# Optimization experiments

Measured on AMD Instinct MI355X. Metric: run time of the kernel, lower is better.

The kernel has to match this reference:

```python
import jax, jax.numpy as jnp
import numpy as np

STRIDES = (8.0, 16.0, 32.0)
ANCHORS = np.array([[[10, 13], [16, 30], [33, 23]],
                    [[30, 61], [62, 45], [59, 119]],
                    [[116, 90], [156, 198], [373, 326]]], dtype=np.float32)
NC = 80
NO = NC + 5
NA = 3
CONF_THRES = 0.15
IOU_THRES = 0.45
MAX_DET = 100
TOPK = 1000          # NMS candidate pre-selection (greedy NMS over top-1000 scores)
MASK_SIZE = 28
MAX_WH = 4096.0      # class offset for batched (class-aware) NMS


def conv(x, w):
    # NCHW conv, stride 1, 'SAME' padding == torch padding=k//2
    return jax.lax.conv_general_dilated(x, w, (1, 1), 'SAME',
                                        dimension_numbers=('NCHW', 'OIHW', 'NCHW'))


def convbn(x, w, g, b, act=False):
    # Conv + (folded) BatchNorm affine + optional SiLU
    y = conv(x, w) * g[None, :, None, None] + b[None, :, None, None]
    return y * jax.nn.sigmoid(y) if act else y


def resize_ac(x, oh, ow):
    # bilinear resize, align_corners=True, NCHW
    H, W = x.shape[-2], x.shape[-1]
    ys = jnp.linspace(0.0, H - 1.0, oh)
    xs = jnp.linspace(0.0, W - 1.0, ow)
    y0 = jnp.floor(ys).astype(jnp.int32); y1 = jnp.minimum(y0 + 1, H - 1)
    x0 = jnp.floor(xs).astype(jnp.int32); x1 = jnp.minimum(x0 + 1, W - 1)
    fy = ys - y0; fx = xs - x0
    rows = x[..., y0, :] * (1.0 - fy)[:, None] + x[..., y1, :] * fy[:, None]
    return rows[..., x0] * (1.0 - fx) + rows[..., x1] * fx


def decode(fraw, anchors_px, stride):
    # fraw: [bs, na*no, ny, nx] -> [bs, na*ny*nx, no] in pixel coords
    bs, _, ny, nx = fraw.shape
    d = fraw.reshape(bs, NA, NO, ny, nx).transpose(0, 1, 3, 4, 2)  # [bs,na,ny,nx,no]
    y = jax.nn.sigmoid(d)
    yv, xv = jnp.meshgrid(jnp.arange(ny, dtype=fraw.dtype),
                          jnp.arange(nx, dtype=fraw.dtype), indexing='ij')
    grid = jnp.stack((xv, yv), -1) - 0.5                 # [ny,nx,2]
    xy = (y[..., :2] * 2.0 + grid) * stride
    wh = (y[..., 2:4] * 2.0) ** 2 * anchors_px[None, :, None, None, :]
    return jnp.concatenate((xy, wh, y[..., 4:]), -1).reshape(bs, -1, NO)


def box_iou(a, b):
    area = lambda t: (t[:, 2] - t[:, 0]) * (t[:, 3] - t[:, 1])
    lt = jnp.maximum(a[:, None, :2], b[None, :, :2])
    rb = jnp.minimum(a[:, None, 2:], b[None, :, 2:])
    wh = jnp.clip(rb - lt, 0.0)
    inter = wh[..., 0] * wh[..., 1]
    return inter / (area(a)[:, None] + area(b)[None, :] - inter + 1e-7)


def nms_image(pred):
    # pred: [N, 85]. conf = obj * cls (multi_label=False -> best class)
    xy = pred[:, :2]; wh = pred[:, 2:4]
    boxes = jnp.concatenate((xy - wh / 2.0, xy + wh / 2.0), -1)
    obj = pred[:, 4]; cls = pred[:, 5:]
    score = obj * jnp.max(cls, -1)
    cls_idx = jnp.argmax(cls, -1)
    s = jnp.where(score > CONF_THRES, score, -1.0)
    sK, idx = jax.lax.top_k(s, TOPK)
    bK = boxes[idx]; cK = cls_idx[idx]
    vK = sK > CONF_THRES
    offb = bK + (cK.astype(bK.dtype) * MAX_WH)[:, None]  # class-aware offset
    iou = box_iou(offb, offb)

    def body(i, st):
        keep, supp = st
        ki = vK[i] & jnp.logical_not(supp[i])
        supp = jnp.where(ki, jnp.logical_or(supp, iou[i] > IOU_THRES), supp)
        return keep.at[i].set(ki), supp

    keep, _ = jax.lax.fori_loop(0, TOPK, body,
                                (jnp.zeros(TOPK, dtype=bool), jnp.zeros(TOPK, dtype=bool)))
    sF = jnp.where(keep, sK, -1.0)
    top_s, top_i = jax.lax.top_k(sF, MAX_DET)
    valid = top_s > 0.0
    out_boxes = bK[top_i] * valid[:, None]
    out_scores = jnp.where(valid, top_s, 0.0)
    out_labels = jnp.where(valid, cK[top_i] + 1, 0)  # 1-based labels
    return out_boxes, out_scores, out_labels, valid


def bilinear_sample(img, ys, xs):
    # img [C,H,W]; ys, xs [P] -> [C,P]; edge-clamped
    H, W = img.shape[-2], img.shape[-1]
    ys = jnp.clip(ys, 0.0, H - 1.0); xs = jnp.clip(xs, 0.0, W - 1.0)
    y0 = jnp.floor(ys).astype(jnp.int32); y1 = jnp.minimum(y0 + 1, H - 1)
    x0 = jnp.floor(xs).astype(jnp.int32); x1 = jnp.minimum(x0 + 1, W - 1)
    ly = ys - y0; lx = xs - x0
    v00 = img[:, y0, x0]; v01 = img[:, y0, x1]
    v10 = img[:, y1, x0]; v11 = img[:, y1, x1]
    return (v00 * (1 - ly) * (1 - lx) + v01 * (1 - ly) * lx +
            v10 * ly * (1 - lx) + v11 * ly * lx)


def roi_align(f, rois, b_idx, out=MASK_SIZE):
    # aligned=False, spatial_scale applied by caller, 1 sample per bin (bin center)
    frac = (jnp.arange(out, dtype=f.dtype) + 0.5) / out

    def one(b, box):
        img = f[b]
        x1, y1, x2, y2 = box[0], box[1], box[2], box[3]
        rw = jnp.maximum(x2 - x1, 1.0); rh = jnp.maximum(y2 - y1, 1.0)
        cx = x1 + frac * rw; cy = y1 + frac * rh
        ys = jnp.repeat(cy, out); xs = jnp.tile(cx, out)
        return bilinear_sample(img, ys, xs).reshape(-1, out, out)

    return jax.vmap(one)(b_idx, rois)


def forward(x0, x1, x2, w_det0, b_det0, w_det1, b_det1, w_det2, b_det2,
            w_seg0, g_seg0, b_seg0, w_seg1, g_seg1, b_seg1, w_seg2, g_seg2, b_seg2,
            w_sc, g_sc, b_sc, w_ml, b_ml):
    feats = (x0, x1, x2)
    wdet = ((w_det0, b_det0), (w_det1, b_det1), (w_det2, b_det2))
    preds = []
    for i in range(3):
        fraw = conv(feats[i], wdet[i][0]) + wdet[i][1][None, :, None, None]
        preds.append(decode(fraw, jnp.asarray(ANCHORS[i]), STRIDES[i]))
    preds = jnp.concatenate(preds, 1)  # [bs, 25200, 85]

    # seg FPN: top-down with align_corners=True bilinear upsample + add
    f = convbn(x2, w_seg0, g_seg0, b_seg0)
    f = resize_ac(f, x1.shape[-2], x1.shape[-1])
    f = convbn(f + x1, w_seg1, g_seg1, b_seg1)
    f = resize_ac(f, x0.shape[-2], x0.shape[-1])
    f = convbn(f + x0, w_seg2, g_seg2, b_seg2)  # [bs, 128, 80, 80]

    boxes, scores, labels, valid = jax.vmap(nms_image)(preds)
    bs = boxes.shape[0]
    rois = jax.lax.stop_gradient(boxes) / STRIDES[0]   # boxes.detach() / stride[0]
    b_idx = jnp.repeat(jnp.arange(bs), MAX_DET)
    crops = roi_align(f, rois.reshape(-1, 4), b_idx)   # [bs*MAX_DET, 128, 28, 28]

    # seg_h: SiLU -> Conv(k=3, act=True) -> 1x1 mask logits
    h = crops * jax.nn.sigmoid(crops)
    h = convbn(h, w_sc, g_sc, b_sc, act=True)
    logits = conv(h, w_ml) + b_ml[None, :, None, None]
    probs = jax.nn.sigmoid(logits)                     # [R, 80, 28, 28]
    lab = jnp.clip(labels.reshape(-1) - 1, 0, NC - 1)  # nc == nc_masks: pick class channel
    masks = probs[jnp.arange(probs.shape[0]), lab]
    masks = masks.reshape(bs, MAX_DET, MASK_SIZE, MASK_SIZE) * valid[..., None, None]
    return boxes, scores, labels, valid, masks


def setup_inputs() -> dict:
    key = jax.random.key(0)
    ks = iter(jax.random.split(key, 48))

    def rn(shape, scale=1.0):
        return jax.random.normal(next(ks), shape, jnp.float32) * scale

    def wconv(o, i, k):
        return rn((o, i, k, k), 1.0 / float(np.sqrt(i * k * k)))

    return {
        'x0': rn((2, 256, 80, 80)),
        'x1': rn((2, 512, 40, 40)),
        'x2': rn((2, 1024, 20, 20)),
        'w_det0': wconv(255, 256, 1), 'b_det0': rn((255,), 0.1),
        'w_det1': wconv(255, 512, 1), 'b_det1': rn((255,), 0.1),
        'w_det2': wconv(255, 1024, 1), 'b_det2': rn((255,), 0.1),
        'w_seg0': wconv(512, 1024, 3), 'g_seg0': jnp.ones(512, jnp.float32), 'b_seg0': rn((512,), 0.1),
        'w_seg1': wconv(256, 512, 3), 'g_seg1': jnp.ones(256, jnp.float32), 'b_seg1': rn((256,), 0.1),
        'w_seg2': wconv(128, 256, 3), 'g_seg2': jnp.ones(128, jnp.float32), 'b_seg2': rn((128,), 0.1),
        'w_sc': wconv(128, 128, 3), 'g_sc': jnp.ones(128, jnp.float32), 'b_sc': rn((128,), 0.1),
        'w_ml': wconv(80, 128, 1), 'b_ml': rn((80,), 0.1),
    }


def reference(x0, x1, x2, w_det0, b_det0, w_det1, b_det1, w_det2, b_det2,
              w_seg0, g_seg0, b_seg0, w_seg1, g_seg1, b_seg1, w_seg2, g_seg2, b_seg2,
              w_sc, g_sc, b_sc, w_ml, b_ml):
    return forward(x0, x1, x2, w_det0, b_det0, w_det1, b_det1, w_det2, b_det2,
                   w_seg0, g_seg0, b_seg0, w_seg1, g_seg1, b_seg1, w_seg2, g_seg2, b_seg2,
                   w_sc, g_sc, b_sc, w_ml, b_ml)
```

## Files before the change

### kernel.cpp

```cpp
#include <hip/hip_runtime.h>
#include <hip/hip_bf16.h>

typedef unsigned int u32;
typedef unsigned long long u64;
typedef short bf16x8 __attribute__((ext_vector_type(8)));
typedef float f32x4 __attribute__((ext_vector_type(4)));

#define NCAND 1000
#define NANCH 25200

__device__ __forceinline__ float sig_acc(float x) { return 1.0f / (1.0f + expf(-x)); }
__device__ __forceinline__ float silu_fast(float v) { return v / (1.0f + __expf(-v)); }
__device__ __forceinline__ unsigned short f2b(float f) {
    __hip_bfloat16 h = __float2bfloat16(f);
    return *reinterpret_cast<unsigned short*>(&h);
}
__device__ __forceinline__ float b2f(unsigned short u) {
    return __uint_as_float(((u32)u) << 16);
}
__device__ __forceinline__ int swz(int p) { return (p & 3) ^ ((p >> 2) & 3); }

__device__ __forceinline__ void gload16(const void* g, void* l) {
    __builtin_amdgcn_global_load_lds((const __attribute__((address_space(1))) void*)g,
                                     (__attribute__((address_space(3))) void*)l, 16, 0, 0);
// ... 70 lines not shown
        }
        __syncthreads();
        for (int k = t; k < 512; k += 256) {
            int pp = k >> 3, cg = k & 7;
            int gp = p0 + pp;
            if (gp < HW) {
                bf16x8 pk;
                #pragma unroll
                for (int j = 0; j < 8; j++) pk[j] = (short)f2b(tile[cg * 8 + j][pp]);
                *(bf16x8*)&y[((size_t)n * HW + gp) * C + c0 + cg * 8] = pk;
            }
        }
    }
}

__global__ __launch_bounds__(256) void det_conv_all_kernel(
    const float* __restrict__ xa, const float* __restrict__ wdta, const float* __restrict__ ba, float* __restrict__ da,
    const float* __restrict__ xb2, const float* __restrict__ wdtb, const float* __restrict__ bb, float* __restrict__ db,
    const float* __restrict__ xc, const float* __restrict__ wdtc, const float* __restrict__ bc, float* __restrict__ dc)
{
    const float* x; const float* wdt; const float* bias; float* dst;
    int C, HW, c_len, nsl, id;
    int blk = blockIdx.x;
    if (blk < 832)       { x = xa;  wdt = wdta; bias = ba; dst = da; C = 256;  HW = 6400; c_len = 256; nsl = 1; id = blk; }
    else if (blk < 1280) { x = xb2; wdt = wdtb; bias = bb; dst = db; C = 512;  HW = 1600; c_len = 256; nsl = 2; id = blk - 832; }
    else                 { x = xc;  wdt = wdtc; bias = bc; dst = dc; C = 1024; HW = 400;  c_len = 128; nsl = 8; id = blk - 1280; }

    int nx = (HW + 127) >> 7;
    int ngroups = nx * nsl * 2;
    int xcd = id & 7;
    int rest = id >> 3;
    int sub = rest & 7;
    int dgrp = rest >> 3;
    int gidx = dgrp * 8 + xcd;
    if (gidx >= ngroups) return;
    int px = gidx % nx;
    int r0 = gidx / nx;
    int slice = r0 % nsl;
    int b = r0 / nsl;
    int oc0 = sub * 32;
    int px0 = px * 128;
    int c0base = slice * c_len;
    __shared__ float xs[2][32][128];
    __shared__ float wsm[2][32][32];
    int t = threadIdx.x;
    int lane = t & 63, wv = t >> 6;
    int pxg = t & 31, og = t >> 5;
    int lpx = pxg << 2;
    bool full = (px0 + 128 <= HW);
    const float* xb = x + (size_t)b * C * HW;

    auto stage = [&](int c0, int nb) {
        if (full) {
            for (int i = wv; i < 16; i += 4) {
                const float* src = xb + (size_t)(c0 + 2 * i + (lane >> 5)) * HW + px0 + (lane & 31) * 4;
                gload16(src, &xs[nb][2 * i][0]);
            }
        } else {
            for (int k = t; k < 4096; k += 256) {
// ... 33 lines not shown
    #pragma unroll
    for (int oo = 0; oo < 4; oo++) {
        int oc = oc0 + (og << 2) + oo;
        if (oc >= 255) continue;
        float bv = (nsl == 1) ? bias[oc] : 0.0f;
        float* ob = outb + ((size_t)b * 255 + oc) * HW;
        if (gp + 3 < HW) {
            float4 v; v.x = acc[oo][0]+bv; v.y = acc[oo][1]+bv; v.z = acc[oo][2]+bv; v.w = acc[oo][3]+bv;
            *(float4*)&ob[gp] = v;
        } else {
            for (int j = 0; j < 4; j++) if (gp + j < HW) ob[gp + j] = acc[oo][j] + bv;
        }
    }
}

__global__ void det_combine_all_kernel(
    const float* __restrict__ p1, const float* __restrict__ b1, float* __restrict__ co1,
    const float* __restrict__ p2, const float* __restrict__ b2, float* __restrict__ co2)
{
    int b = blockIdx.x, t = threadIdx.x;
    const float* parts; const float* bias; float* co; int nsl, HW, tid, total4;
    if (b < 797) { parts = p1; bias = b1; co = co1; nsl = 2; HW = 1600; tid = b * 256 + t; total4 = 2 * 255 * 1600 / 4; }
    else         { parts = p2; bias = b2; co = co2; nsl = 8; HW = 400;  tid = (b - 797) * 256 + t; total4 = 2 * 255 * 400 / 4; }
    if (tid >= total4) return;
    size_t stride = (size_t)2 * 255 * HW;
    float4 s = {0.f, 0.f, 0.f, 0.f};
    for (int sl = 0; sl < nsl; sl++) {
        float4 v = *(const float4*)&parts[sl * stride + (size_t)tid * 4];
        s.x += v.x; s.y += v.y; s.z += v.z; s.w += v.w;
    }
    int oc = ((tid * 4) / HW) % 255;
    float bv = bias[oc];
    s.x += bv; s.y += bv; s.z += bv; s.w += bv;
    *(float4*)&co[(size_t)tid * 4] = s;
}

__global__ void decode_all_kernel(const float* __restrict__ co0, const float* __restrict__ co1,
    const float* __restrict__ co2, float* __restrict__ boxes_all, u64* __restrict__ keys,
    int* __restrict__ cls_all)
{
    int blk = blockIdx.x, t = threadIdx.x;
    const float* conv; int ny, base, total; float stride;
    float aw0, ah0, aw1, ah1, aw2, ah2;
    int tid;
    if (blk < 150) {
        conv = co0; ny = 80; stride = 8.0f; base = 0; total = 38400;
        aw0 = 10.f; ah0 = 13.f; aw1 = 16.f; ah1 = 30.f; aw2 = 33.f; ah2 = 23.f;
        tid = blk * 256 + t;
    } else if (blk < 188) {
        conv = co1; ny = 40; stride = 16.0f; base = 19200; total = 9600;
        aw0 = 30.f; ah0 = 61.f; aw1 = 62.f; ah1 = 45.f; aw2 = 59.f; ah2 = 119.f;
        tid = (blk - 150) * 256 + t;
    } else {
        conv = co2; ny = 20; stride = 32.0f; base = 24000; total = 2400;
        aw0 = 116.f; ah0 = 90.f; aw1 = 156.f; ah1 = 198.f; aw2 = 373.f; ah2 = 326.f;
        tid = (blk - 188) * 256 + t;
    }
    if (tid >= total) return;
    int nx = ny;
    int HW = ny * nx;
    int gx = tid % nx; int r = tid / nx;
    int gy = r % ny; r /= ny;
    int a = r % 3; int b = r / 3;
    const float* cb = conv + ((size_t)b * 255 + a * 85) * HW + (size_t)gy * nx + gx;
    float v0 = cb[0];
    float v1 = cb[(size_t)1 * HW];
    float v2 = cb[(size_t)2 * HW];
    float v3 = cb[(size_t)3 * HW];
    float v4 = cb[(size_t)4 * HW];
    float mx = cb[(size_t)5 * HW];
    int mi = 0;
    for (int o = 6; o < 85; o++) {
        float q = cb[(size_t)o * HW];
        if (q > mx) { mx = q; mi = o - 5; }
    }
    float aw = (a == 0) ? aw0 : ((a == 1) ? aw1 : aw2);
    float ah = (a == 0) ? ah0 : ((a == 1) ? ah1 : ah2);
    float sx = sig_acc(v0), sy = sig_acc(v1);
    float sw2 = 2.0f * sig_acc(v2), sh2 = 2.0f * sig_acc(v3);
    float cx = (2.0f * sx + ((float)gx - 0.5f)) * stride;
    float cy = (2.0f * sy + ((float)gy - 0.5f)) * stride;
    float bw = sw2 * sw2 * aw;
    float bh = sh2 * sh2 * ah;
    float score = sig_acc(v4) * sig_acc(mx);
    float s = (score > 0.15f) ? score : -1.0f;
    u32 fb = __float_as_uint(s);
    u32 m = (fb & 0x80000000u) ? ~fb : (fb | 0x80000000u);
    int gidx = base + (a * ny + gy) * nx + gx;
    size_t gi = (size_t)b * NANCH + gidx;
    float4 bx;
    bx.x = cx - bw * 0.5f; bx.y = cy - bh * 0.5f;
    bx.z = cx + bw * 0.5f; bx.w = cy + bh * 0.5f;
    *(float4*)&boxes_all[gi * 4] = bx;
    keys[gi] = ((u64)m << 32) | (u64)(0xFFFFFFFFu - (u32)gidx);
    cls_all[gi] = mi;
}

#define XBUF 21504
__device__ __forceinline__ void conv3x3_body(int id, char* smem,
    const unsigned short* __restrict__ in, const unsigned short* __restrict__ wp,
    const float* __restrict__ gain, const float* __restrict__ bias,
    unsigned short* __restrict__ out, const float* __restrict__ zerobuf,
    int Cin, int Cout, int H, int W, int act, int ksl, float* __restrict__ pout)
{
    bool on = (threadIdx.x < 256);
    int tilesX = (W + 15) >> 4;
    int tilesY = (H + 15) >> 4;
    int tiles = tilesX * tilesY;
    int nocb = Cout >> 6;
    int ngroups = tiles * ksl * 2;
    int xcd = id & 7;
    int rest = id >> 3;
    int sub = rest % nocb;
// ... 106 lines not shown
                *(f32x4*)&ob[(q << 4) + (lg << 2)] = acc[p][q];
        }
    }
}

__global__ __launch_bounds__(256) void mfma_conv3x3(
    const unsigned short* __restrict__ in, const unsigned short* __restrict__ wp,
    const float* __restrict__ gain, const float* __restrict__ bias,
    unsigned short* __restrict__ out, const float* __restrict__ zerobuf,
    int Cin, int Cout, int H, int W, int act, int ksl, float* __restrict__ pout)
{
    __shared__ __align__(16) char smem[2 * XBUF];
    conv3x3_body(blockIdx.x, smem, in, wp, gain, bias, out, zerobuf, Cin, Cout, H, W, act, ksl, pout);
}

union TKU { u32 h[4][2048]; u64 sortb[2048]; };

__global__ __launch_bounds__(1024) void topk_seg0_kernel(
    const u64* __restrict__ keys_all, const float* __restrict__ boxes_all,
    const int* __restrict__ cls_all,
    float* __restrict__ cbox, float* __restrict__ coff,
    float* __restrict__ cscore, int* __restrict__ ccls,
    const unsigned short* __restrict__ x2n, const unsigned short* __restrict__ wp0,
    const float* __restrict__ g_seg0, const float* __restrict__ b_seg0,
    unsigned short* __restrict__ f0, const float* __restrict__ zerobuf,
    float* __restrict__ pbuf)
{
    __shared__ __align__(16) char ms[2 * XBUF];
    __shared__ u32 s_prefix;
    __shared__ int s_rank, s_bin, s_cntgt;
    __shared__ u32 s_cnt;
    if (blockIdx.x >= 2) {
        conv3x3_body((int)blockIdx.x - 2, ms, x2n, wp0, g_seg0, b_seg0, f0, zerobuf,
                     1024, 512, 20, 20, 0, 4, pbuf);
        return;
    }
    TKU& sh = *(TKU*)ms;
    int img = blockIdx.x;
    const u64* keys = keys_all + (size_t)img * NANCH;
    int t = threadIdx.x;
    if (t == 0) { s_prefix = 0; s_rank = NCAND; }
    __syncthreads();
    u32 maskdone = 0;
    #pragma unroll 1
    for (int pass = 0; pass < 3; pass++) {
        int shift = (pass == 0) ? 21 : ((pass == 1) ? 10 : 0);
        int nbins = (pass == 2) ? 1024 : 2048;
        for (int i = t; i < 4 * 2048; i += 1024) ((u32*)sh.h)[i] = 0;
        __syncthreads();
        u32 pfx = s_prefix;
        for (int i = t; i < NANCH; i += 1024) {
            u32 u = (u32)(keys[i] >> 32);
            if ((u & maskdone) == pfx) atomicAdd(&sh.h[t & 3][(u >> shift) & (nbins - 1)], 1u);
        }
        __syncthreads();
        for (int i = t; i < nbins; i += 1024)
            sh.h[0][i] = sh.h[0][i] + sh.h[1][i] + sh.h[2][i] + sh.h[3][i];
        __syncthreads();
        u32* A = sh.h[0]; u32* B = sh.h[1];
        for (int st = 1; st < nbins; st <<= 1) {
            for (int i = t; i < nbins; i += 1024)
                B[i] = A[i] + ((i + st < nbins) ? A[i + st] : 0u);
            __syncthreads();
            u32* tmp = A; A = B; B = tmp;
        }
        int rk = s_rank;
        for (int i = t; i < nbins; i += 1024) {
            u32 ge = A[i];
            u32 gt = (i + 1 < nbins) ? A[i + 1] : 0u;
            if (ge >= (u32)rk && gt < (u32)rk) { s_bin = i; s_cntgt = (int)gt; }
        }
        __syncthreads();
        if (t == 0) {
            s_prefix |= ((u32)s_bin) << shift;
            s_rank -= s_cntgt;
        }
        maskdone |= (u32)(nbins - 1) << shift;
        __syncthreads();
    }
    u32 pivot = s_prefix;
    if (t == 0) s_cnt = 0;
    __syncthreads();
    for (int i = t; i < NANCH; i += 1024) {
        u64 k = keys[i]; u32 u = (u32)(k >> 32);
        if (u > pivot) { u32 p = atomicAdd(&s_cnt, 1u); sh.sortb[p] = k; }
    }
    __syncthreads();
    for (int i = t; i < NANCH; i += 1024) {
        u64 k = keys[i]; u32 u = (u32)(k >> 32);
        if (u == pivot) { u32 p = atomicAdd(&s_cnt, 1u); if (p < 2048) sh.sortb[p] = k; }
    }
    __syncthreads();
    u32 nc = s_cnt; if (nc > 2048) nc = 2048;
    for (int i = t; i < 2048; i += 1024) if ((u32)i >= nc) sh.sortb[i] = 0ull;
    __syncthreads();
    for (int k = 2; k <= 2048; k <<= 1) {
        for (int j = k >> 1; j > 0; j >>= 1) {
            __syncthreads();
            for (int i = t; i < 2048; i += 1024) {
                int ixj = i ^ j;
                if (ixj > i) {
                    u64 a = sh.sortb[i], c = sh.sortb[ixj];
                    bool first = ((i & k) == 0);
                    if (first ? (a < c) : (a > c)) { sh.sortb[i] = c; sh.sortb[ixj] = a; }
                }
            }
        }
    }
    __syncthreads();
    for (int i = t; i < NCAND; i += 1024) {
        u64 k = sh.sortb[i];
        u32 u = (u32)(k >> 32);
        u32 fb = (u & 0x80000000u) ? (u ^ 0x80000000u) : ~u;
        float s = __uint_as_float(fb);
        int idx = (int)(0xFFFFFFFFu - (u32)k);
        size_t gi = (size_t)img * NANCH + idx;
        float4 bx = *(const float4*)&boxes_all[gi * 4];
        int cl = cls_all[gi];
        int o = img * NCAND + i;
        *(float4*)&cbox[(size_t)o * 4] = bx;
        float off = (float)cl * 4096.0f;
        float4 ob; ob.x = bx.x + off; ob.y = bx.y + off; ob.z = bx.z + off; ob.w = bx.w + off;
        *(float4*)&coff[(size_t)o * 4] = ob;
        cscore[o] = s;
        ccls[o] = cl;
    }
}

__device__ __forceinline__ void seg_combine_body(int tid, const float* __restrict__ parts,
    const float* __restrict__ gain, const float* __restrict__ bias,
    unsigned short* __restrict__ out, int nsl, int total4, int C, int act)
{
    if (tid >= total4) return;
    size_t stride = (size_t)total4 * 4;
    float4 s = {0.f, 0.f, 0.f, 0.f};
    for (int sl = 0; sl < nsl; sl++) {
        float4 v = *(const float4*)&parts[sl * stride + (size_t)tid * 4];
        s.x += v.x; s.y += v.y; s.z += v.z; s.w += v.w;
    }
    int oc = (tid * 4) % C;
    float r[4] = {s.x, s.y, s.z, s.w};
// ... 2 lines not shown
    for (int j = 0; j < 4; j++) {
        float v = r[j] * gain[oc + j] + bias[oc + j];
        if (act) v = silu_fast(v);
        ((unsigned short*)&pk)[j] = f2b(v);
    }
    *(ushort4*)&out[(size_t)tid * 4] = pk;
}

__global__ void seg_combine_kernel(const float* __restrict__ parts,
    const float* __restrict__ gain, const float* __restrict__ bias,
    unsigned short* __restrict__ out, int nsl, int total4, int C, int act)
{
    seg_combine_body(blockIdx.x * 256 + threadIdx.x, parts, gain, bias, out, nsl, total4, C, act);
}

__global__ __launch_bounds__(256) void nmsmask_comb0_kernel(
    const float* __restrict__ coff, u64* __restrict__ maskbuf,
    const float* __restrict__ parts, const float* __restrict__ gain,
    const float* __restrict__ bias, unsigned short* __restrict__ outb)
{
    int blk = blockIdx.x, t = threadIdx.x;
    if (blk >= 126) {
        seg_combine_body((blk - 126) * 256 + t, parts, gain, bias, outb, 4, 2*400*512/4, 512, 0);
        return;
    }
    int img = blk / 63;
    int tid = (blk % 63) * 256 + t;
    if (tid >= NCAND * 16) return;
    int i = tid >> 4, jw = tid & 15;
    const float* cb = coff + (size_t)img * NCAND * 4;
    float ax1 = cb[i*4+0], ay1 = cb[i*4+1], ax2 = cb[i*4+2], ay2 = cb[i*4+3];
    float aarea = (ax2 - ax1) * (ay2 - ay1);
    u64 bits = 0;
    for (int jj = 0; jj < 64; jj++) {
        int j = jw * 64 + jj;
        if (j >= NCAND) break;
        float bx1 = cb[j*4+0], by1 = cb[j*4+1], bx2 = cb[j*4+2], by2 = cb[j*4+3];
        float barea = (bx2 - bx1) * (by2 - by1);
        float ltx = fmaxf(ax1, bx1), lty = fmaxf(ay1, by1);
        float rbx = fminf(ax2, bx2), rby = fminf(ay2, by2);
        float ww = fmaxf(rbx - ltx, 0.0f), hh = fmaxf(rby - lty, 0.0f);
        float inter = ww * hh;
        float iou = inter / (aarea + barea - inter + 1e-7f);
        if (iou > 0.45f) bits |= (1ull << jj);
    }
    maskbuf[((size_t)img * 1024 + i) * 16 + jw] = bits;
}

__device__ __forceinline__ void resize_add_body(int tid, const unsigned short* __restrict__ f,
    const unsigned short* __restrict__ skip, unsigned short* __restrict__ out,
    int C8, int C, int IH, int IW, int OH, int OW)
{
    int total = 2 * OH * OW * C8;
    if (tid >= total) return;
    int cg = tid % C8; int r = tid / C8;
    int ox = r % OW; r /= OW;
    int oy = r % OH; int n = r / OH;
    float sy = (float)(IH - 1) / (float)(OH - 1);
    float sx = (float)(IW - 1) / (float)(OW - 1);
    float ys = oy * sy, xs = ox * sx;
    int y0 = (int)floorf(ys); if (y0 > IH - 1) y0 = IH - 1;
// ... 5 lines not shown
    bf16x8 a01 = *(const bf16x8*)&fb[(size_t)(y0 * IW + x1) * C];
    bf16x8 a10 = *(const bf16x8*)&fb[(size_t)(y1 * IW + x0) * C];
    bf16x8 a11 = *(const bf16x8*)&fb[(size_t)(y1 * IW + x1) * C];
    bf16x8 sk = *(const bf16x8*)&skip[(size_t)tid * 8];
    bf16x8 o;
    #pragma unroll
    for (int j = 0; j < 8; j++) {
        float r0 = b2f((unsigned short)a00[j]) * (1.0f - fy) + b2f((unsigned short)a10[j]) * fy;
        float r1 = b2f((unsigned short)a01[j]) * (1.0f - fy) + b2f((unsigned short)a11[j]) * fy;
        float v = r0 * (1.0f - fx) + r1 * fx + b2f((unsigned short)sk[j]);
        o[j] = (short)f2b(v);
    }
    *(bf16x8*)&out[(size_t)tid * 8] = o;
}

__global__ void resize_add_kernel(const unsigned short* __restrict__ f,
    const unsigned short* __restrict__ skip, unsigned short* __restrict__ out,
    int C8, int C, int IH, int IW, int OH, int OW)
{
    resize_add_body(blockIdx.x * 256 + threadIdx.x, f, skip, out, C8, C, IH, IW, OH, OW);
}

__global__ __launch_bounds__(256) void nmsserial_resize1_kernel(
    const float* __restrict__ cbox, const float* __restrict__ cscore,
    const int* __restrict__ ccls, const u64* __restrict__ maskbuf,
    float* __restrict__ out, float* __restrict__ rois,
    int* __restrict__ lab, float* __restrict__ validf,
    const unsigned short* __restrict__ f0, const unsigned short* __restrict__ x1n,
    unsigned short* __restrict__ r1b)
{
    __shared__ float sS[1024];
    int t = threadIdx.x;
    if (blockIdx.x >= 2) {
        resize_add_body(((int)blockIdx.x - 2) * 256 + t, f0, x1n, r1b, 64, 512, 20, 20, 40, 40);
        return;
    }
    int img = blockIdx.x;
    for (int i = t; i < 1024; i += 256)
        sS[i] = (i < NCAND) ? cscore[img * NCAND + i] : -1.0f;
    __syncthreads();
    if (t >= 64) return;
    int lane = t;
    u64 validw = 0;
    #pragma unroll
    for (int w = 0; w < 16; w++) {
        u64 b = __ballot(sS[w * 64 + lane] > 0.15f);
        if (lane == w) validw = b;
    }
    const u64* mrow = maskbuf + (size_t)img * 1024 * 16;
// ... 272 lines not shown
    float* coffb  = (float*)alloc((size_t)2 * NCAND * 4 * 4);
    float* cscore = (float*)alloc((size_t)2 * NCAND * 4);
    int*   ccls   = (int*)  alloc((size_t)2 * NCAND * 4);
    u64*   maskb  = (u64*)  alloc((size_t)2 * 1024 * 16 * 8);
    float* wdt0   = (float*)alloc((size_t)256 * 256 * 4);
    float* wdt1   = (float*)alloc((size_t)512 * 256 * 4);
    float* wdt2   = (float*)alloc((size_t)1024 * 256 * 4);
    unsigned short* x0n = (unsigned short*)alloc((size_t)2 * 6400 * 256 * 2);
    unsigned short* x1n = (unsigned short*)alloc((size_t)2 * 1600 * 512 * 2);
    unsigned short* x2n = (unsigned short*)alloc((size_t)2 * 400 * 1024 * 2);
    const size_t s0 = (size_t)512 * 1024 * 9, s1 = (size_t)256 * 512 * 9,
                 s2 = (size_t)128 * 256 * 9,  s3 = (size_t)128 * 128 * 9;
    unsigned short* wprep = (unsigned short*)alloc((s0 + s1 + s2 + s3) * 2);
    float* pbuf = (float*)alloc((size_t)4 * 2 * 1600 * 256 * 4);
    float* pbuf2 = pbuf + (size_t)2 * 2 * 255 * 1600;
    unsigned short* f0   = (unsigned short*)alloc((size_t)2 * 400 * 512 * 2);
    unsigned short* r1b  = (unsigned short*)alloc((size_t)2 * 1600 * 512 * 2);
    unsigned short* f1   = (unsigned short*)alloc((size_t)2 * 1600 * 256 * 2);
    unsigned short* r2b  = (unsigned short*)alloc((size_t)2 * 6400 * 256 * 2);
    unsigned short* fseg = (unsigned short*)alloc((size_t)2 * 6400 * 128 * 2);
    float* zerobuf = (float*)alloc(2048);
    float* roisW  = (float*)alloc((size_t)200 * 4 * 4);
    int*   labW   = (int*)  alloc((size_t)200 * 4);
    float* validW = (float*)alloc((size_t)200 * 4);
    float* pdot   = (float*)alloc((size_t)4 * 200 * 784 * 4);
    unsigned short* hbuf   = (unsigned short*)alloc((size_t)200 * 784 * 128 * 2);

    int DCH = 200;
    if (off > ws_size) {
        DCH = 25;
        hbuf = (unsigned short*)co0;
    }

    prep_all_kernel<<<4289, 256, 0, stream>>>(
        w_det0, w_det1, w_det2, wdt0, wdt1, wdt2,
        w_seg0, w_seg1, w_seg2, w_sc,
        wprep, wprep + s0, wprep + s0 + s1, wprep + s0 + s1 + s2,
        x0, x1, x2, x0n, x1n, x2n, zerobuf);

    det_conv_all_kernel<<<1792, 256, 0, stream>>>(
        x0, wdt0, b_det0, co0,
        x1, wdt1, b_det1, pbuf,
        x2, wdt2, b_det2, pbuf2);

    det_combine_all_kernel<<<997, 256, 0, stream>>>(pbuf, b_det1, co1, pbuf2, b_det2, co2);

    decode_all_kernel<<<198, 256, 0, stream>>>(co0, co1, co2, boxesA, keysA, clsA);

    topk_seg0_kernel<<<258, 1024, 0, stream>>>(keysA, boxesA, clsA,
        cbox, coffb, cscore, ccls,
        x2n, wprep, g_seg0, b_seg0, f0, zerobuf, pbuf);

    nmsmask_comb0_kernel<<<526, 256, 0, stream>>>(coffb, maskb,
        pbuf, g_seg0, b_seg0, f0);

    nmsserial_resize1_kernel<<<802, 256, 0, stream>>>(cbox, cscore, ccls, maskb,
        out, roisW, labW, validW, f0, x1n, r1b);

    mfma_conv3x3<<<288, 256, 0, stream>>>(r1b, wprep + s0, g_seg1, b_seg1, f1, zerobuf, 512, 256, 40, 40, 0, 4, pbuf);
    seg_combine_kernel<<<800, 256, 0, stream>>>(pbuf, g_seg1, b_seg1, f1, 4, 2*1600*256/4, 256, 0);
    resize_add_kernel<<<1600, 256, 0, stream>>>(f1, x0n, r2b, 32, 256, 40, 40, 80, 80);
    mfma_conv3x3<<<208, 256, 0, stream>>>(r2b, wprep + s0 + s1, g_seg2, b_seg2, fseg, zerobuf, 256, 128, 80, 80, 0, 2, pbuf);
    seg_combine_kernel<<<1600, 256, 0, stream>>>(pbuf, g_seg2, b_seg2, fseg, 2, 2*6400*128/4, 128, 0);

    for (int d0i = 0; d0i < 200; d0i += DCH) {
        int total = DCH * 784 * 16;
        roi_silu_kernel<<<(total + 255) / 256, 256, 0, stream>>>(fseg, roisW, validW, d0i, total, hbuf);
        mfma_conv_mask<<<DCH * 16, 256, 0, stream>>>(hbuf, wprep + s0 + s1 + s2,
            g_sc, b_sc, w_ml, labW, validW, d0i, pdot, zerobuf);
    }
    mask_combine_kernel<<<(200 * 784 + 255) / 256, 256, 0, stream>>>(pdot, b_ml, labW, validW, out);
}
```

Measured before the change: 380.6 us.

## Reschedule seg-branch stages into detection kernels to cut launches and overlap work

Restructures the cross-stage schedule so each segmentation stage runs one step earlier, packed into the same launch as an independent detection/NMS stage. The seg0 conv is merged with the det convs, seg0 combine with the det combine, and resize1 with decode. Seg1 conv then shares a launch with top-k, seg1 combine with the NMS mask, and resize2 with serial NMS. This removes three launches and fills idle CUs during the serial top-k and NMS blocks. It costs a separate partial-sum buffer for seg0, and the heterogeneous blocks may compete for resources.

```diff
diff --git a/kernel.cpp b/kernel.cpp
--- a/kernel.cpp
+++ b/kernel.cpp
@@ -108,18 +108,15 @@
     }
 }
 
-__global__ __launch_bounds__(256) void det_conv_all_kernel(
-    const float* __restrict__ xa, const float* __restrict__ wdta, const float* __restrict__ ba, float* __restrict__ da,
-    const float* __restrict__ xb2, const float* __restrict__ wdtb, const float* __restrict__ bb, float* __restrict__ db,
-    const float* __restrict__ xc, const float* __restrict__ wdtc, const float* __restrict__ bc, float* __restrict__ dc)
-{
-    const float* x; const float* wdt; const float* bias; float* dst;
-    int C, HW, c_len, nsl, id;
-    int blk = blockIdx.x;
-    if (blk < 832)       { x = xa;  wdt = wdta; bias = ba; dst = da; C = 256;  HW = 6400; c_len = 256; nsl = 1; id = blk; }
-    else if (blk < 1280) { x = xb2; wdt = wdtb; bias = bb; dst = db; C = 512;  HW = 1600; c_len = 256; nsl = 2; id = blk - 832; }
-    else                 { x = xc;  wdt = wdtc; bias = bc; dst = dc; C = 1024; HW = 400;  c_len = 128; nsl = 8; id = blk - 1280; }
-
+#define XBUF 21504
+__device__ __forceinline__ void det_conv_body(int id, char* smembase,
+    const float* __restrict__ x, const float* __restrict__ wdt, const float* __restrict__ bias,
+    float* __restrict__ dst, int C, int HW, int c_len, int nsl)
+{
+    typedef float XS[32][128];
+    typedef float WS[32][32];
+    XS* xs = (XS*)smembase;
+    WS* wsm = (WS*)(smembase + 32768);
     int nx = (HW + 127) >> 7;
     int ngroups = nx * nsl * 2;
     int xcd = id & 7;
@@ -135,8 +132,6 @@
     int oc0 = sub * 32;
     int px0 = px * 128;
     int c0base = slice * c_len;
-    __shared__ float xs[2][32][128];
-    __shared__ float wsm[2][32][32];
     int t = threadIdx.x;
     int lane = t & 63, wv = t >> 6;
     int pxg = t & 31, og = t >> 5;
@@ -200,89 +195,6 @@
     }
 }
 
-__global__ void det_combine_all_kernel(
-    const float* __restrict__ p1, const float* __restrict__ b1, float* __restrict__ co1,
-    const float* __restrict__ p2, const float* __restrict__ b2, float* __restrict__ co2)
-{
-    int b = blockIdx.x, t = threadIdx.x;
-    const float* parts; const float* bias; float* co; int nsl, HW, tid, total4;
-    if (b < 797) { parts = p1; bias = b1; co = co1; nsl = 2; HW = 1600; tid = b * 256 + t; total4 = 2 * 255 * 1600 / 4; }
-    else         { parts = p2; bias = b2; co = co2; nsl = 8; HW = 400;  tid = (b - 797) * 256 + t; total4 = 2 * 255 * 400 / 4; }
-    if (tid >= total4) return;
-    size_t stride = (size_t)2 * 255 * HW;
-    float4 s = {0.f, 0.f, 0.f, 0.f};
-    for (int sl = 0; sl < nsl; sl++) {
-        float4 v = *(const float4*)&parts[sl * stride + (size_t)tid * 4];
-        s.x += v.x; s.y += v.y; s.z += v.z; s.w += v.w;
-    }
-    int oc = ((tid * 4) / HW) % 255;
-    float bv = bias[oc];
-    s.x += bv; s.y += bv; s.z += bv; s.w += bv;
-    *(float4*)&co[(size_t)tid * 4] = s;
-}
-
-__global__ void decode_all_kernel(const float* __restrict__ co0, const float* __restrict__ co1,
-    const float* __restrict__ co2, float* __restrict__ boxes_all, u64* __restrict__ keys,
-    int* __restrict__ cls_all)
-{
-    int blk = blockIdx.x, t = threadIdx.x;
-    const float* conv; int ny, base, total; float stride;
-    float aw0, ah0, aw1, ah1, aw2, ah2;
-    int tid;
-    if (blk < 150) {
-        conv = co0; ny = 80; stride = 8.0f; base = 0; total = 38400;
-        aw0 = 10.f; ah0 = 13.f; aw1 = 16.f; ah1 = 30.f; aw2 = 33.f; ah2 = 23.f;
-        tid = blk * 256 + t;
-    } else if (blk < 188) {
-        conv = co1; ny = 40; stride = 16.0f; base = 19200; total = 9600;
-        aw0 = 30.f; ah0 = 61.f; aw1 = 62.f; ah1 = 45.f; aw2 = 59.f; ah2 = 119.f;
-        tid = (blk - 150) * 256 + t;
-    } else {
-        conv = co2; ny = 20; stride = 32.0f; base = 24000; total = 2400;
-        aw0 = 116.f; ah0 = 90.f; aw1 = 156.f; ah1 = 198.f; aw2 = 373.f; ah2 = 326.f;
-        tid = (blk - 188) * 256 + t;
-    }
-    if (tid >= total) return;
-    int nx = ny;
-    int HW = ny * nx;
-    int gx = tid % nx; int r = tid / nx;
-    int gy = r % ny; r /= ny;
-    int a = r % 3; int b = r / 3;
-    const float* cb = conv + ((size_t)b * 255 + a * 85) * HW + (size_t)gy * nx + gx;
-    float v0 = cb[0];
-    float v1 = cb[(size_t)1 * HW];
-    float v2 = cb[(size_t)2 * HW];
-    float v3 = cb[(size_t)3 * HW];
-    float v4 = cb[(size_t)4 * HW];
-    float mx = cb[(size_t)5 * HW];
-    int mi = 0;
-    for (int o = 6; o < 85; o++) {
-        float q = cb[(size_t)o * HW];
-        if (q > mx) { mx = q; mi = o - 5; }
-    }
-    float aw = (a == 0) ? aw0 : ((a == 1) ? aw1 : aw2);
-    float ah = (a == 0) ? ah0 : ((a == 1) ? ah1 : ah2);
-    float sx = sig_acc(v0), sy = sig_acc(v1);
-    float sw2 = 2.0f * sig_acc(v2), sh2 = 2.0f * sig_acc(v3);
-    float cx = (2.0f * sx + ((float)gx - 0.5f)) * stride;
-    float cy = (2.0f * sy + ((float)gy - 0.5f)) * stride;
-    float bw = sw2 * sw2 * aw;
-    float bh = sh2 * sh2 * ah;
-    float score = sig_acc(v4) * sig_acc(mx);
-    float s = (score > 0.15f) ? score : -1.0f;
-    u32 fb = __float_as_uint(s);
-    u32 m = (fb & 0x80000000u) ? ~fb : (fb | 0x80000000u);
-    int gidx = base + (a * ny + gy) * nx + gx;
-    size_t gi = (size_t)b * NANCH + gidx;
-    float4 bx;
-    bx.x = cx - bw * 0.5f; bx.y = cy - bh * 0.5f;
-    bx.z = cx + bw * 0.5f; bx.w = cy + bh * 0.5f;
-    *(float4*)&boxes_all[gi * 4] = bx;
-    keys[gi] = ((u64)m << 32) | (u64)(0xFFFFFFFFu - (u32)gidx);
-    cls_all[gi] = mi;
-}
-
-#define XBUF 21504
 __device__ __forceinline__ void conv3x3_body(int id, char* smem,
     const unsigned short* __restrict__ in, const unsigned short* __restrict__ wp,
     const float* __restrict__ gain, const float* __restrict__ bias,
@@ -419,117 +331,20 @@
     conv3x3_body(blockIdx.x, smem, in, wp, gain, bias, out, zerobuf, Cin, Cout, H, W, act, ksl, pout);
 }
 
-union TKU { u32 h[4][2048]; u64 sortb[2048]; };
-
-__global__ __launch_bounds__(1024) void topk_seg0_kernel(
-    const u64* __restrict__ keys_all, const float* __restrict__ boxes_all,
-    const int* __restrict__ cls_all,
-    float* __restrict__ cbox, float* __restrict__ coff,
-    float* __restrict__ cscore, int* __restrict__ ccls,
+__global__ __launch_bounds__(256) void detseg_conv_kernel(
+    const float* __restrict__ xa, const float* __restrict__ wdta, const float* __restrict__ ba, float* __restrict__ da,
+    const float* __restrict__ xb2, const float* __restrict__ wdtb, const float* __restrict__ bb, float* __restrict__ db,
+    const float* __restrict__ xc, const float* __restrict__ wdtc, const float* __restrict__ bc, float* __restrict__ dc,
     const unsigned short* __restrict__ x2n, const unsigned short* __restrict__ wp0,
     const float* __restrict__ g_seg0, const float* __restrict__ b_seg0,
-    unsigned short* __restrict__ f0, const float* __restrict__ zerobuf,
-    float* __restrict__ pbuf)
-{
-    __shared__ __align__(16) char ms[2 * XBUF];
-    __shared__ u32 s_prefix;
-    __shared__ int s_rank, s_bin, s_cntgt;
-    __shared__ u32 s_cnt;
-    if (blockIdx.x >= 2) {
-        conv3x3_body((int)blockIdx.x - 2, ms, x2n, wp0, g_seg0, b_seg0, f0, zerobuf,
-                     1024, 512, 20, 20, 0, 4, pbuf);
-        return;
-    }
-    TKU& sh = *(TKU*)ms;
-    int img = blockIdx.x;
-    const u64* keys = keys_all + (size_t)img * NANCH;
-    int t = threadIdx.x;
-    if (t == 0) { s_prefix = 0; s_rank = NCAND; }
-    __syncthreads();
-    u32 maskdone = 0;
-    #pragma unroll 1
-    for (int pass = 0; pass < 3; pass++) {
-        int shift = (pass == 0) ? 21 : ((pass == 1) ? 10 : 0);
-        int nbins = (pass == 2) ? 1024 : 2048;
-        for (int i = t; i < 4 * 2048; i += 1024) ((u32*)sh.h)[i] = 0;
-        __syncthreads();
-        u32 pfx = s_prefix;
-        for (int i = t; i < NANCH; i += 1024) {
-            u32 u = (u32)(keys[i] >> 32);
-            if ((u & maskdone) == pfx) atomicAdd(&sh.h[t & 3][(u >> shift) & (nbins - 1)], 1u);
-        }
-        __syncthreads();
-        for (int i = t; i < nbins; i += 1024)
-            sh.h[0][i] = sh.h[0][i] + sh.h[1][i] + sh.h[2][i] + sh.h[3][i];
-        __syncthreads();
-        u32* A = sh.h[0]; u32* B = sh.h[1];
-        for (int st = 1; st < nbins; st <<= 1) {
-            for (int i = t; i < nbins; i += 1024)
-                B[i] = A[i] + ((i + st < nbins) ? A[i + st] : 0u);
-            __syncthreads();
-            u32* tmp = A; A = B; B = tmp;
-        }
-        int rk = s_rank;
-        for (int i = t; i < nbins; i += 1024) {
-            u32 ge = A[i];
-            u32 gt = (i + 1 < nbins) ? A[i + 1] : 0u;
-            if (ge >= (u32)rk && gt < (u32)rk) { s_bin = i; s_cntgt = (int)gt; }
-        }
-        __syncthreads();
-        if (t == 0) {
-            s_prefix |= ((u32)s_bin) << shift;
-            s_rank -= s_cntgt;
-        }
-        maskdone |= (u32)(nbins - 1) << shift;
-        __syncthreads();
-    }
-    u32 pivot = s_prefix;
-    if (t == 0) s_cnt = 0;
-    __syncthreads();
-    for (int i = t; i < NANCH; i += 1024) {
-        u64 k = keys[i]; u32 u = (u32)(k >> 32);
-        if (u > pivot) { u32 p = atomicAdd(&s_cnt, 1u); sh.sortb[p] = k; }
-    }
-    __syncthreads();
-    for (int i = t; i < NANCH; i += 1024) {
-        u64 k = keys[i]; u32 u = (u32)(k >> 32);
-        if (u == pivot) { u32 p = atomicAdd(&s_cnt, 1u); if (p < 2048) sh.sortb[p] = k; }
-    }
-    __syncthreads();
-    u32 nc = s_cnt; if (nc > 2048) nc = 2048;
-    for (int i = t; i < 2048; i += 1024) if ((u32)i >= nc) sh.sortb[i] = 0ull;
-    __syncthreads();
-    for (int k = 2; k <= 2048; k <<= 1) {
-        for (int j = k >> 1; j > 0; j >>= 1) {
-            __syncthreads();
-            for (int i = t; i < 2048; i += 1024) {
-                int ixj = i ^ j;
-                if (ixj > i) {
-                    u64 a = sh.sortb[i], c = sh.sortb[ixj];
-                    bool first = ((i & k) == 0);
-                    if (first ? (a < c) : (a > c)) { sh.sortb[i] = c; sh.sortb[ixj] = a; }
-                }
-            }
-        }
-    }
-    __syncthreads();
-    for (int i = t; i < NCAND; i += 1024) {
-        u64 k = sh.sortb[i];
-        u32 u = (u32)(k >> 32);
-        u32 fb = (u & 0x80000000u) ? (u ^ 0x80000000u) : ~u;
-        float s = __uint_as_float(fb);
-        int idx = (int)(0xFFFFFFFFu - (u32)k);
-        size_t gi = (size_t)img * NANCH + idx;
-        float4 bx = *(const float4*)&boxes_all[gi * 4];
-        int cl = cls_all[gi];
-        int o = img * NCAND + i;
-        *(float4*)&cbox[(size_t)o * 4] = bx;
-        float off = (float)cl * 4096.0f;
-        float4 ob; ob.x = bx.x + off; ob.y = bx.y + off; ob.z = bx.z + off; ob.w = bx.w + off;
-        *(float4*)&coff[(size_t)o * 4] = ob;
-        cscore[o] = s;
-        ccls[o] = cl;
-    }
+    unsigned short* __restrict__ f0, const float* __restrict__ zerobuf, float* __restrict__ segp0)
+{
+    __shared__ __align__(16) char smem[2 * XBUF];
+    int blk = blockIdx.x;
+    if (blk < 832)       det_conv_body(blk, smem, xa, wdta, ba, da, 256, 6400, 256, 1);
+    else if (blk < 1280) det_conv_body(blk - 832, smem, xb2, wdtb, bb, db, 512, 1600, 256, 2);
+    else if (blk < 1792) det_conv_body(blk - 1280, smem, xc, wdtc, bc, dc, 1024, 400, 128, 8);
+    else conv3x3_body(blk - 1792, smem, x2n, wp0, g_seg0, b_seg0, f0, zerobuf, 1024, 512, 20, 20, 0, 4, segp0);
 }
 
 __device__ __forceinline__ void seg_combine_body(int tid, const float* __restrict__ parts,
@@ -562,37 +377,31 @@
     seg_combine_body(blockIdx.x * 256 + threadIdx.x, parts, gain, bias, out, nsl, total4, C, act);
 }
 
-__global__ __launch_bounds__(256) void nmsmask_comb0_kernel(
-    const float* __restrict__ coff, u64* __restrict__ maskbuf,
-    const float* __restrict__ parts, const float* __restrict__ gain,
-    const float* __restrict__ bias, unsigned short* __restrict__ outb)
-{
-    int blk = blockIdx.x, t = threadIdx.x;
-    if (blk >= 126) {
-        seg_combine_body((blk - 126) * 256 + t, parts, gain, bias, outb, 4, 2*400*512/4, 512, 0);
+__global__ void combine_both_kernel(
+    const float* __restrict__ p1, const float* __restrict__ b1, float* __restrict__ co1,
+    const float* __restrict__ p2, const float* __restrict__ b2, float* __restrict__ co2,
+    const float* __restrict__ segp0, const float* __restrict__ g_seg0,
+    const float* __restrict__ b_seg0, unsigned short* __restrict__ f0)
+{
+    int b = blockIdx.x, t = threadIdx.x;
+    if (b >= 997) {
+        seg_combine_body((b - 997) * 256 + t, segp0, g_seg0, b_seg0, f0, 4, 2*400*512/4, 512, 0);
         return;
     }
-    int img = blk / 63;
-    int tid = (blk % 63) * 256 + t;
-    if (tid >= NCAND * 16) return;
-    int i = tid >> 4, jw = tid & 15;
-    const float* cb = coff + (size_t)img * NCAND * 4;
-    float ax1 = cb[i*4+0], ay1 = cb[i*4+1], ax2 = cb[i*4+2], ay2 = cb[i*4+3];
-    float aarea = (ax2 - ax1) * (ay2 - ay1);
-    u64 bits = 0;
-    for (int jj = 0; jj < 64; jj++) {
-        int j = jw * 64 + jj;
-        if (j >= NCAND) break;
-        float bx1 = cb[j*4+0], by1 = cb[j*4+1], bx2 = cb[j*4+2], by2 = cb[j*4+3];
-        float barea = (bx2 - bx1) * (by2 - by1);
-        float ltx = fmaxf(ax1, bx1), lty = fmaxf(ay1, by1);
-        float rbx = fminf(ax2, bx2), rby = fminf(ay2, by2);
-        float ww = fmaxf(rbx - ltx, 0.0f), hh = fmaxf(rby - lty, 0.0f);
-        float inter = ww * hh;
-        float iou = inter / (aarea + barea - inter + 1e-7f);
-        if (iou > 0.45f) bits |= (1ull << jj);
-    }
-    maskbuf[((size_t)img * 1024 + i) * 16 + jw] = bits;
+    const float* parts; const float* bias; float* co; int nsl, HW, tid, total4;
+    if (b < 797) { parts = p1; bias = b1; co = co1; nsl = 2; HW = 1600; tid = b * 256 + t; total4 = 2 * 255 * 1600 / 4; }
+    else         { parts = p2; bias = b2; co = co2; nsl = 8; HW = 400;  tid = (b - 797) * 256 + t; total4 = 2 * 255 * 400 / 4; }
+    if (tid >= total4) return;
+    size_t stride = (size_t)2 * 255 * HW;
+    float4 s = {0.f, 0.f, 0.f, 0.f};
+    for (int sl = 0; sl < nsl; sl++) {
+        float4 v = *(const float4*)&parts[sl * stride + (size_t)tid * 4];
+        s.x += v.x; s.y += v.y; s.z += v.z; s.w += v.w;
+    }
+    int oc = ((tid * 4) / HW) % 255;
+    float bv = bias[oc];
+    s.x += bv; s.y += bv; s.z += bv; s.w += bv;
+    *(float4*)&co[(size_t)tid * 4] = s;
 }
 
 __device__ __forceinline__ void resize_add_body(int tid, const unsigned short* __restrict__ f,
@@ -628,25 +437,231 @@
     *(bf16x8*)&out[(size_t)tid * 8] = o;
 }
 
-__global__ void resize_add_kernel(const unsigned short* __restrict__ f,
-    const unsigned short* __restrict__ skip, unsigned short* __restrict__ out,
-    int C8, int C, int IH, int IW, int OH, int OW)
-{
-    resize_add_body(blockIdx.x * 256 + threadIdx.x, f, skip, out, C8, C, IH, IW, OH, OW);
-}
-
-__global__ __launch_bounds__(256) void nmsserial_resize1_kernel(
+__global__ void decode_resize1_kernel(const float* __restrict__ co0, const float* __restrict__ co1,
+    const float* __restrict__ co2, float* __restrict__ boxes_all, u64* __restrict__ keys,
+    int* __restrict__ cls_all,
+    const unsigned short* __restrict__ f0, const unsigned short* __restrict__ x1n,
+    unsigned short* __restrict__ r1b)
+{
+    int blk = blockIdx.x, t = threadIdx.x;
+    if (blk >= 198) {
+        resize_add_body((blk - 198) * 256 + t, f0, x1n, r1b, 64, 512, 20, 20, 40, 40);
+        return;
+    }
+    const float* conv; int ny, base, total; float stride;
+    float aw0, ah0, aw1, ah1, aw2, ah2;
+    int tid;
+    if (blk < 150) {
+        conv = co0; ny = 80; stride = 8.0f; base = 0; total = 38400;
+        aw0 = 10.f; ah0 = 13.f; aw1 = 16.f; ah1 = 30.f; aw2 = 33.f; ah2 = 23.f;
+        tid = blk * 256 + t;
+    } else if (blk < 188) {
+        conv = co1; ny = 40; stride = 16.0f; base = 19200; total = 9600;
+        aw0 = 30.f; ah0 = 61.f; aw1 = 62.f; ah1 = 45.f; aw2 = 59.f; ah2 = 119.f;
+        tid = (blk - 150) * 256 + t;
+    } else {
+        conv = co2; ny = 20; stride = 32.0f; base = 24000; total = 2400;
+        aw0 = 116.f; ah0 = 90.f; aw1 = 156.f; ah1 = 198.f; aw2 = 373.f; ah2 = 326.f;
+        tid = (blk - 188) * 256 + t;
+    }
+    if (tid >= total) return;
+    int nx = ny;
+    int HW = ny * nx;
+    int gx = tid % nx; int r = tid / nx;
+    int gy = r % ny; r /= ny;
+    int a = r % 3; int b = r / 3;
+    const float* cb = conv + ((size_t)b * 255 + a * 85) * HW + (size_t)gy * nx + gx;
+    float v0 = cb[0];
+    float v1 = cb[(size_t)1 * HW];
+    float v2 = cb[(size_t)2 * HW];
+    float v3 = cb[(size_t)3 * HW];
+    float v4 = cb[(size_t)4 * HW];
+    float mx = cb[(size_t)5 * HW];
+    int mi = 0;
+    for (int o = 6; o < 85; o++) {
+        float q = cb[(size_t)o * HW];
+        if (q > mx) { mx = q; mi = o - 5; }
+    }
+    float aw = (a == 0) ? aw0 : ((a == 1) ? aw1 : aw2);
+    float ah = (a == 0) ? ah0 : ((a == 1) ? ah1 : ah2);
+    float sx = sig_acc(v0), sy = sig_acc(v1);
+    float sw2 = 2.0f * sig_acc(v2), sh2 = 2.0f * sig_acc(v3);
+    float cx = (2.0f * sx + ((float)gx - 0.5f)) * stride;
+    float cy = (2.0f * sy + ((float)gy - 0.5f)) * stride;
+    float bw = sw2 * sw2 * aw;
+    float bh = sh2 * sh2 * ah;
+    float score = sig_acc(v4) * sig_acc(mx);
+    float s = (score > 0.15f) ? score : -1.0f;
+    u32 fb = __float_as_uint(s);
+    u32 m = (fb & 0x80000000u) ? ~fb : (fb | 0x80000000u);
+    int gidx = base + (a * ny + gy) * nx + gx;
+    size_t gi = (size_t)b * NANCH + gidx;
+    float4 bx;
+    bx.x = cx - bw * 0.5f; bx.y = cy - bh * 0.5f;
+    bx.z = cx + bw * 0.5f; bx.w = cy + bh * 0.5f;
+    *(float4*)&boxes_all[gi * 4] = bx;
+    keys[gi] = ((u64)m << 32) | (u64)(0xFFFFFFFFu - (u32)gidx);
+    cls_all[gi] = mi;
+}
+
+union TKU { u32 h[4][2048]; u64 sortb[2048]; };
+
+__global__ __launch_bounds__(1024) void topk_seg1_kernel(
+    const u64* __restrict__ keys_all, const float* __restrict__ boxes_all,
+    const int* __restrict__ cls_all,
+    float* __restrict__ cbox, float* __restrict__ coff,
+    float* __restrict__ cscore, int* __restrict__ ccls,
+    const unsigned short* __restrict__ r1b, const unsigned short* __restrict__ wp1,
+    const float* __restrict__ g_seg1, const float* __restrict__ b_seg1,
+    unsigned short* __restrict__ f1, const float* __restrict__ zerobuf,
+    float* __restrict__ pbuf)
+{
+    __shared__ __align__(16) char ms[2 * XBUF];
+    __shared__ u32 s_prefix;
+    __shared__ int s_rank, s_bin, s_cntgt;
+    __shared__ u32 s_cnt;
+    if (blockIdx.x >= 2) {
+        conv3x3_body((int)blockIdx.x - 2, ms, r1b, wp1, g_seg1, b_seg1, f1, zerobuf,
+                     512, 256, 40, 40, 0, 4, pbuf);
+        return;
+    }
+    TKU& sh = *(TKU*)ms;
+    int img = blockIdx.x;
+    const u64* keys = keys_all + (size_t)img * NANCH;
+    int t = threadIdx.x;
+    if (t == 0) { s_prefix = 0; s_rank = NCAND; }
+    __syncthreads();
+    u32 maskdone = 0;
+    #pragma unroll 1
+    for (int pass = 0; pass < 3; pass++) {
+        int shift = (pass == 0) ? 21 : ((pass == 1) ? 10 : 0);
+        int nbins = (pass == 2) ? 1024 : 2048;
+        for (int i = t; i < 4 * 2048; i += 1024) ((u32*)sh.h)[i] = 0;
+        __syncthreads();
+        u32 pfx = s_prefix;
+        for (int i = t; i < NANCH; i += 1024) {
+            u32 u = (u32)(keys[i] >> 32);
+            if ((u & maskdone) == pfx) atomicAdd(&sh.h[t & 3][(u >> shift) & (nbins - 1)], 1u);
+        }
+        __syncthreads();
+        for (int i = t; i < nbins; i += 1024)
+            sh.h[0][i] = sh.h[0][i] + sh.h[1][i] + sh.h[2][i] + sh.h[3][i];
+        __syncthreads();
+        u32* A = sh.h[0]; u32* B = sh.h[1];
+        for (int st = 1; st < nbins; st <<= 1) {
+            for (int i = t; i < nbins; i += 1024)
+                B[i] = A[i] + ((i + st < nbins) ? A[i + st] : 0u);
+            __syncthreads();
+            u32* tmp = A; A = B; B = tmp;
+        }
+        int rk = s_rank;
+        for (int i = t; i < nbins; i += 1024) {
+            u32 ge = A[i];
+            u32 gt = (i + 1 < nbins) ? A[i + 1] : 0u;
+            if (ge >= (u32)rk && gt < (u32)rk) { s_bin = i; s_cntgt = (int)gt; }
+        }
+        __syncthreads();
+        if (t == 0) {
+            s_prefix |= ((u32)s_bin) << shift;
+            s_rank -= s_cntgt;
+        }
+        maskdone |= (u32)(nbins - 1) << shift;
+        __syncthreads();
+    }
+    u32 pivot = s_prefix;
+    if (t == 0) s_cnt = 0;
+    __syncthreads();
+    for (int i = t; i < NANCH; i += 1024) {
+        u64 k = keys[i]; u32 u = (u32)(k >> 32);
+        if (u > pivot) { u32 p = atomicAdd(&s_cnt, 1u); sh.sortb[p] = k; }
+    }
+    __syncthreads();
+    for (int i = t; i < NANCH; i += 1024) {
+        u64 k = keys[i]; u32 u = (u32)(k >> 32);
+        if (u == pivot) { u32 p = atomicAdd(&s_cnt, 1u); if (p < 2048) sh.sortb[p] = k; }
+    }
+    __syncthreads();
+    u32 nc = s_cnt; if (nc > 2048) nc = 2048;
+    for (int i = t; i < 2048; i += 1024) if ((u32)i >= nc) sh.sortb[i] = 0ull;
+    __syncthreads();
+    for (int k = 2; k <= 2048; k <<= 1) {
+        for (int j = k >> 1; j > 0; j >>= 1) {
+            __syncthreads();
+            for (int i = t; i < 2048; i += 1024) {
+                int ixj = i ^ j;
+                if (ixj > i) {
+                    u64 a = sh.sortb[i], c = sh.sortb[ixj];
+                    bool first = ((i & k) == 0);
+                    if (first ? (a < c) : (a > c)) { sh.sortb[i] = c; sh.sortb[ixj] = a; }
+                }
+            }
+        }
+    }
+    __syncthreads();
+    for (int i = t; i < NCAND; i += 1024) {
+        u64 k = sh.sortb[i];
+        u32 u = (u32)(k >> 32);
+        u32 fb = (u & 0x80000000u) ? (u ^ 0x80000000u) : ~u;
+        float s = __uint_as_float(fb);
+        int idx = (int)(0xFFFFFFFFu - (u32)k);
+        size_t gi = (size_t)img * NANCH + idx;
+        float4 bx = *(const float4*)&boxes_all[gi * 4];
+        int cl = cls_all[gi];
+        int o = img * NCAND + i;
+        *(float4*)&cbox[(size_t)o * 4] = bx;
+        float off = (float)cl * 4096.0f;
+        float4 ob; ob.x = bx.x + off; ob.y = bx.y + off; ob.z = bx.z + off; ob.w = bx.w + off;
+        *(float4*)&coff[(size_t)o * 4] = ob;
+        cscore[o] = s;
+        ccls[o] = cl;
+    }
+}
+
+__global__ __launch_bounds__(256) void nmsmask_comb1_kernel(
+    const float* __restrict__ coff, u64* __restrict__ maskbuf,
+    const float* __restrict__ parts, const float* __restrict__ gain,
+    const float* __restrict__ bias, unsigned short* __restrict__ outb)
+{
+    int blk = blockIdx.x, t = threadIdx.x;
+    if (blk >= 126) {
+        seg_combine_body((blk - 126) * 256 + t, parts, gain, bias, outb, 4, 2*1600*256/4, 256, 0);
+        return;
+    }
+    int img = blk / 63;
+    int tid = (blk % 63) * 256 + t;
+    if (tid >= NCAND * 16) return;
+    int i = tid >> 4, jw = tid & 15;
+    const float* cb = coff + (size_t)img * NCAND * 4;
+    float ax1 = cb[i*4+0], ay1 = cb[i*4+1], ax2 = cb[i*4+2], ay2 = cb[i*4+3];
+    float aarea = (ax2 - ax1) * (ay2 - ay1);
+    u64 bits = 0;
+    for (int jj = 0; jj < 64; jj++) {
+        int j = jw * 64 + jj;
+        if (j >= NCAND) break;
+        float bx1 = cb[j*4+0], by1 = cb[j*4+1], bx2 = cb[j*4+2], by2 = cb[j*4+3];
+        float barea = (bx2 - bx1) * (by2 - by1);
+        float ltx = fmaxf(ax1, bx1), lty = fmaxf(ay1, by1);
+        float rbx = fminf(ax2, bx2), rby = fminf(ay2, by2);
+        float ww = fmaxf(rbx - ltx, 0.0f), hh = fmaxf(rby - lty, 0.0f);
+        float inter = ww * hh;
+        float iou = inter / (aarea + barea - inter + 1e-7f);
+        if (iou > 0.45f) bits |= (1ull << jj);
+    }
+    maskbuf[((size_t)img * 1024 + i) * 16 + jw] = bits;
+}
+
+__global__ __launch_bounds__(256) void nmsserial_resize2_kernel(
     const float* __restrict__ cbox, const float* __restrict__ cscore,
     const int* __restrict__ ccls, const u64* __restrict__ maskbuf,
     float* __restrict__ out, float* __restrict__ rois,
     int* __restrict__ lab, float* __restrict__ validf,
-    const unsigned short* __restrict__ f0, const unsigned short* __restrict__ x1n,
-    unsigned short* __restrict__ r1b)
+    const unsigned short* __restrict__ f1, const unsigned short* __restrict__ x0n,
+    unsigned short* __restrict__ r2b)
 {
     __shared__ float sS[1024];
     int t = threadIdx.x;
     if (blockIdx.x >= 2) {
-        resize_add_body(((int)blockIdx.x - 2) * 256 + t, f0, x1n, r1b, 64, 512, 20, 20, 40, 40);
+        resize_add_body(((int)blockIdx.x - 2) * 256 + t, f1, x0n, r2b, 32, 256, 40, 40, 80, 80);
         return;
     }
     int img = blockIdx.x;
@@ -949,6 +964,7 @@
     unsigned short* wprep = (unsigned short*)alloc((s0 + s1 + s2 + s3) * 2);
     float* pbuf = (float*)alloc((size_t)4 * 2 * 1600 * 256 * 4);
     float* pbuf2 = pbuf + (size_t)2 * 2 * 255 * 1600;
+    float* segp0 = (float*)alloc((size_t)4 * 2 * 400 * 512 * 4);
     unsigned short* f0   = (unsigned short*)alloc((size_t)2 * 400 * 512 * 2);
     unsigned short* r1b  = (unsigned short*)alloc((size_t)2 * 1600 * 512 * 2);
     unsigned short* f1   = (unsigned short*)alloc((size_t)2 * 1600 * 256 * 2);
@@ -973,28 +989,28 @@
         wprep, wprep + s0, wprep + s0 + s1, wprep + s0 + s1 + s2,
         x0, x1, x2, x0n, x1n, x2n, zerobuf);
 
-    det_conv_all_kernel<<<1792, 256, 0, stream>>>(
+    detseg_conv_kernel<<<2048, 256, 0, stream>>>(
         x0, wdt0, b_det0, co0,
         x1, wdt1, b_det1, pbuf,
-        x2, wdt2, b_det2, pbuf2);
-
-    det_combine_all_kernel<<<997, 256, 0, stream>>>(pbuf, b_det1, co1, pbuf2, b_det2, co2);
-
-    decode_all_kernel<<<198, 256, 0, stream>>>(co0, co1, co2, boxesA, keysA, clsA);
-
-    topk_seg0_kernel<<<258, 1024, 0, stream>>>(keysA, boxesA, clsA,
+        x2, wdt2, b_det2, pbuf2,
+        x2n, wprep, g_seg0, b_seg0, f0, zerobuf, segp0);
+
+    combine_both_kernel<<<1397, 256, 0, stream>>>(pbuf, b_det1, co1, pbuf2, b_det2, co2,
+                                                  segp0, g_seg0, b_seg0, f0);
+
+    decode_resize1_kernel<<<998, 256, 0, stream>>>(co0, co1, co2, boxesA, keysA, clsA,
+                                                   f0, x1n, r1b);
+
+    topk_seg1_kernel<<<290, 1024, 0, stream>>>(keysA, boxesA, clsA,
         cbox, coffb, cscore, ccls,
-        x2n, wprep, g_seg0, b_seg0, f0, zerobuf, pbuf);
-
-    nmsmask_comb0_kernel<<<526, 256, 0, stream>>>(coffb, maskb,
-        pbuf, g_seg0, b_seg0, f0);
-
-    nmsserial_resize1_kernel<<<802, 256, 0, stream>>>(cbox, cscore, ccls, maskb,
-        out, roisW, labW, validW, f0, x1n, r1b);
-
-    mfma_conv3x3<<<288, 256, 0, stream>>>(r1b, wprep + s0, g_seg1, b_seg1, f1, zerobuf, 512, 256, 40, 40, 0, 4, pbuf);
-    seg_combine_kernel<<<800, 256, 0, stream>>>(pbuf, g_seg1, b_seg1, f1, 4, 2*1600*256/4, 256, 0);
-    resize_add_kernel<<<1600, 256, 0, stream>>>(f1, x0n, r2b, 32, 256, 40, 40, 80, 80);
+        r1b, wprep + s0, g_seg1, b_seg1, f1, zerobuf, pbuf);
+
+    nmsmask_comb1_kernel<<<926, 256, 0, stream>>>(coffb, maskb,
+        pbuf, g_seg1, b_seg1, f1);
+
+    nmsserial_resize2_kernel<<<1602, 256, 0, stream>>>(cbox, cscore, ccls, maskb,
+        out, roisW, labW, validW, f1, x0n, r2b);
+
     mfma_conv3x3<<<208, 256, 0, stream>>>(r2b, wprep + s0 + s1, g_seg2, b_seg2, fseg, zerobuf, 256, 128, 80, 80, 0, 2, pbuf);
     seg_combine_kernel<<<1600, 256, 0, stream>>>(pbuf, g_seg2, b_seg2, fseg, 2, 2*6400*128/4, 128, 0);
 
```

Measured after the change: 366.1 us. -3.8%, faster.
